# Kernel optimization log

Measured on AMD Instinct MI355X. Metric: run time of the kernel, lower is better.

Reference implementation:

```python
import jax, jax.numpy as jnp
import numpy as np

B, S, SK = 4, 256, 512
D, NH, NKV, HD = 1024, 16, 4, 64
DE, NE = 4096, 8
LANG_CODES = jnp.arange(4, 4 + NE)  # expert language codes (codes > 3 are routed)
LN_EPS = 1e-5


def setup_inputs() -> dict:
    key = jax.random.key(0)
    ks = jax.random.split(key, 32)
    sc = 0.02
    n = lambda k, shape: jax.random.normal(k, shape, jnp.float32)
    causal = jnp.where(jnp.tril(jnp.ones((S, S), bool)), 0.0, -1e9).astype(jnp.float32)
    inp = {
        "hidden_states": n(ks[0], (B, S, D)),
        "encoder_hidden_states": n(ks[1], (B, SK, D)),
        "attention_mask": jnp.broadcast_to(causal, (B, 1, S, S)),
        "encoder_attention_mask": jnp.zeros((B, 1, S, SK), jnp.float32),
        "langs": jax.random.randint(ks[2], (B, 2), 0, 12),
        "ln1_g": jnp.ones((D,), jnp.float32), "ln1_b": jnp.zeros((D,), jnp.float32),
        "sa_q_w": n(ks[3], (D, D)) * sc, "sa_q_b": jnp.zeros((D,), jnp.float32),
        "sa_k_w": n(ks[4], (D, NKV * HD)) * sc, "sa_k_b": jnp.zeros((NKV * HD,), jnp.float32),
        "sa_v_w": n(ks[5], (D, NKV * HD)) * sc, "sa_v_b": jnp.zeros((NKV * HD,), jnp.float32),
        "sa_o_w": n(ks[6], (D, D)) * sc, "sa_o_b": jnp.zeros((D,), jnp.float32),
        "ln2_g": jnp.ones((D,), jnp.float32), "ln2_b": jnp.zeros((D,), jnp.float32),
        "ca_q_w": n(ks[7], (D, D)) * sc, "ca_q_b": jnp.zeros((D,), jnp.float32),
        "ca_k_w": n(ks[8], (D, NKV * HD)) * sc, "ca_k_b": jnp.zeros((NKV * HD,), jnp.float32),
        "ca_v_w": n(ks[9], (D, NKV * HD)) * sc, "ca_v_b": jnp.zeros((NKV * HD,), jnp.float32),
        "ca_o_w": n(ks[10], (D, D)) * sc, "ca_o_b": jnp.zeros((D,), jnp.float32),
        "ln3_g": jnp.ones((D,), jnp.float32), "ln3_b": jnp.zeros((D,), jnp.float32),
        "moe_w1": n(ks[11], (NE, D, DE)) * sc,
        "moe_w2": n(ks[12], (NE, DE, D)) * sc,
        "moe_w3": n(ks[13], (NE, D, DE)) * sc,
    }
    return inp


def _ln(x, g, b):
    m = jnp.mean(x, -1, keepdims=True)
    v = jnp.var(x, -1, keepdims=True)
    return (x - m) * jax.lax.rsqrt(v + LN_EPS) * g + b


def _gqa(x, kv, qw, qb, kw, kb, vw, vb, ow, ob, mask):
    b, sq, _ = x.shape
    skv = kv.shape[1]
    q = ((x @ qw + qb) * HD ** -0.5).reshape(b, sq, NH, HD)
    k = (kv @ kw + kb).reshape(b, skv, NKV, HD)
    v = (kv @ vw + vb).reshape(b, skv, NKV, HD)
    rep = NH // NKV
    k = jnp.repeat(k, rep, axis=2)  # head h = kv_head*rep + r, matches repeat_kv
    v = jnp.repeat(v, rep, axis=2)
    scores = jnp.einsum('bqhd,bkhd->bhqk', q, k) + mask
    p = jax.nn.softmax(scores, axis=-1)
    o = jnp.einsum('bhqk,bkhd->bqhd', p, v).reshape(b, sq, NH * HD)
    return o @ ow + ob


def _moe(x, w1, w2, w3, langs):
    # routing: weight 1/(# lang codes > 3) per sequence; 1 if none
    counts = jnp.sum(langs > 3, axis=-1)
    rw = jnp.where(counts == 0, 1.0, 1.0 / jnp.maximum(counts, 1).astype(x.dtype))  # [B]
    match = jnp.any(langs[None, :, :] == LANG_CODES[:, None, None], axis=-1)  # [E,B]
    coef = match.astype(x.dtype) * rw[None, :]  # [E,B]
    h = jax.nn.gelu(jnp.einsum('bsd,edf->ebsf', x, w1), approximate=False) \
        * jnp.einsum('bsd,edf->ebsf', x, w3)
    out = jnp.einsum('ebsf,efd->ebsd', h, w2)
    return jnp.einsum('ebsd,eb->bsd', out, coef)


def reference(hidden_states, encoder_hidden_states, attention_mask, encoder_attention_mask,
              langs, ln1_g, ln1_b, sa_q_w, sa_q_b, sa_k_w, sa_k_b, sa_v_w, sa_v_b,
              sa_o_w, sa_o_b, ln2_g, ln2_b, ca_q_w, ca_q_b, ca_k_w, ca_k_b, ca_v_w,
              ca_v_b, ca_o_w, ca_o_b, ln3_g, ln3_b, moe_w1, moe_w2, moe_w3):
    # self attention (causal GQA, prefill, pre-LN)
    r = hidden_states
    h = _ln(hidden_states, ln1_g, ln1_b)
    h = _gqa(h, h, sa_q_w, sa_q_b, sa_k_w, sa_k_b, sa_v_w, sa_v_b, sa_o_w, sa_o_b,
             attention_mask)
    h = r + h
    # cross attention over encoder states
    r = h
    h = _ln(h, ln2_g, ln2_b)
    h = _gqa(h, encoder_hidden_states, ca_q_w, ca_q_b, ca_k_w, ca_k_b, ca_v_w, ca_v_b,
             ca_o_w, ca_o_b, encoder_attention_mask)
    h = r + h
    # language-routed MoE FFN
    r = h
    h = _ln(h, ln3_g, ln3_b)
    h = _moe(h, moe_w1, moe_w2, moe_w3, langs)
    return r + h
```

## Files before the change

### kernel.cpp

```cpp
#include <hip/hip_runtime.h>
#include <math.h>

#define B_   4
#define S_   256
#define SK_  512
#define D_   1024
#define NH_  16
#define NKV_ 4
#define HD_  64
#define DE_  4096
#define NE_  8

typedef __attribute__((ext_vector_type(8))) short bf16x8;
typedef __attribute__((ext_vector_type(4))) float f32x4;

struct __align__(8) s4 { short x, y, z, w; };

#define MFMA(a,b,c) __builtin_amdgcn_mfma_f32_16x16x32_bf16(a,b,c,0,0,0)

__device__ __forceinline__ unsigned short f2b(float f) {
  union { float f; unsigned u; } v; v.f = f;
  unsigned r = v.u + 0x7FFF + ((v.u >> 16) & 1);
  return (unsigned short)(r >> 16);
}

__device__ __forceinline__ unsigned short f2bh(float f) {
  return (unsigned short)((__float_as_uint(f) + 0x8000u) >> 16);
}

__device__ __forceinline__ void tconv_tile(float (*T)[65],
                                           const float* __restrict__ W,
                                           short* __restrict__ Wt,
                                           int N, int K, int n0, int k0) {
  int t = threadIdx.x;
  int kk = t >> 4, n4 = (t & 15) * 4;
#pragma unroll
  for (int it = 0; it < 4; ++it) {
    float4 v = *(const float4*)(W + (size_t)(k0 + kk + 16 * it) * N + n0 + n4);
    T[kk + 16 * it][n4 + 0] = v.x;
    T[kk + 16 * it][n4 + 1] = v.y;
    T[kk + 16 * it][n4 + 2] = v.z;
    T[kk + 16 * it][n4 + 3] = v.w;
  }
  __syncthreads();
  int n = t >> 2, kb = (t & 3) * 16;
  bf16x8 o0, o1;
#pragma unroll
  for (int j = 0; j < 8; ++j) o0[j] = (short)f2bh(T[kb + j][n]);
#pragma unroll
  for (int j = 0; j < 8; ++j) o1[j] = (short)f2bh(T[kb + 8 + j][n]);
  short* dst = Wt + (size_t)(n0 + n) * K + k0 + kb;
  *(bf16x8*)dst = o0;
  *(bf16x8*)(dst + 8) = o1;
}

struct P8 {
  const float* s[8];
  short* d[8];
  int n[8];
};

__global__ __launch_bounds__(256) void tconv_attn(P8 p) {
  int z = blockIdx.z;
  int N = p.n[z];
  if ((int)blockIdx.x * 64 >= N) return;
  __shared__ float T[64][65];
  tconv_tile(T, p.s[z], p.d[z], N, D_, blockIdx.x * 64, blockIdx.y * 64);
}

__global__ __launch_bounds__(256) void tconv_moe(const float* __restrict__ w1,
                                                 const float* __restrict__ w3,
                                                 const float* __restrict__ w2,
                                                 short* __restrict__ w1t,
                                                 short* __restrict__ w3t,
                                                 short* __restrict__ w2t,
                                                 const int* __restrict__ eact) {
  int z = blockIdx.z;
  int e = z / 3, m = z - e * 3;
  if (!eact[e]) return;
  __shared__ float T[64][65];
  size_t off = (size_t)e * D_ * DE_;
  if (m == 0) {
    tconv_tile(T, w1 + off, w1t + off, DE_, D_, blockIdx.x * 64, blockIdx.y * 64);
  } else if (m == 1) {
    tconv_tile(T, w3 + off, w3t + off, DE_, D_, blockIdx.x * 64, blockIdx.y * 64);
  } else {
    int lin = blockIdx.y * 64 + blockIdx.x;
    int nt = lin & 15, kt = lin >> 4;
    tconv_tile(T, w2 + off, w2t + off, D_, DE_, nt * 64, kt * 64);
  }
}

__global__ __launch_bounds__(256) void ln_kernel(const float* __restrict__ x,
                                                 const float* __restrict__ g,
                                                 const float* __restrict__ be,
                                                 short* __restrict__ y) {
  int row = blockIdx.x, tid = threadIdx.x;
  const float4 v = ((const float4*)(x + (size_t)row * D_))[tid];
  float s  = v.x + v.y + v.z + v.w;
  float s2 = v.x*v.x + v.y*v.y + v.z*v.z + v.w*v.w;
  __shared__ float r1[256], r2[256];
  r1[tid] = s; r2[tid] = s2; __syncthreads();
  for (int off = 128; off > 0; off >>= 1) {
    if (tid < off) { r1[tid] += r1[tid+off]; r2[tid] += r2[tid+off]; }
    __syncthreads();
  }
  float mean = r1[0] * (1.0f / D_);
  float var  = r2[0] * (1.0f / D_) - mean * mean;
  float inv  = rsqrtf(var + 1e-5f);
  int c = tid * 4;
  s4 o;
  o.x = (short)f2b((v.x - mean) * inv * g[c]   + be[c]);
  o.y = (short)f2b((v.y - mean) * inv * g[c+1] + be[c+1]);
  o.z = (short)f2b((v.z - mean) * inv * g[c+2] + be[c+2]);
  o.w = (short)f2b((v.w - mean) * inv * g[c+3] + be[c+3]);
  *(s4*)(y + (size_t)row * D_ + c) = o;
}

__global__ void cast_f2b(const float* __restrict__ in, short* __restrict__ out, int n) {
  int i = (blockIdx.x * 256 + threadIdx.x) * 4;
  if (i < n) {
    float4 v = *(const float4*)(in + i);
    s4 o; o.x=(short)f2b(v.x); o.y=(short)f2b(v.y); o.z=(short)f2b(v.z); o.w=(short)f2b(v.w);
    *(s4*)(out + i) = o;
  }
}

__global__ __launch_bounds__(256) void proj_mfma(const short* __restrict__ A,
                                                 const short* __restrict__ Wt,
                                                 const float* __restrict__ bias,
                                                 short* __restrict__ Cb,
                                                 float scale, int N, int K) {
  int bn = blockIdx.x * 64, bm = blockIdx.y * 64;
  int lane = threadIdx.x & 63, wv = threadIdx.x >> 6;
  int wm = (wv & 1) * 32, wn = (wv >> 1) * 32;
  int quad = lane >> 4, l16 = lane & 15;
  f32x4 z4 = {0.f,0.f,0.f,0.f};
  f32x4 acc[2][2] = {{z4,z4},{z4,z4}};
  const short* a0p = A + (size_t)(bm + wm + l16) * K;
  const short* a1p = a0p + (size_t)16 * K;
  const short* w0p = Wt + (size_t)(bn + wn + l16) * K;
  const short* w1p = w0p + (size_t)16 * K;
#pragma unroll 2
  for (int k0 = 0; k0 < K; k0 += 32) {
    int ka = k0 + quad * 8;
    bf16x8 a0 = *(const bf16x8*)(a0p + ka);
    bf16x8 a1 = *(const bf16x8*)(a1p + ka);
    bf16x8 b0 = *(const bf16x8*)(w0p + ka);
    bf16x8 b1 = *(const bf16x8*)(w1p + ka);
    acc[0][0] = MFMA(a0, b0, acc[0][0]);
    acc[0][1] = MFMA(a0, b1, acc[0][1]);
    acc[1][0] = MFMA(a1, b0, acc[1][0]);
    acc[1][1] = MFMA(a1, b1, acc[1][1]);
  }
#pragma unroll
  for (int i = 0; i < 2; ++i)
#pragma unroll
    for (int j = 0; j < 2; ++j) {
      int n = bn + wn + j*16 + l16;
      float bs = bias[n];
#pragma unroll
      for (int r = 0; r < 4; ++r) {
        int m = bm + wm + i*16 + quad*4 + r;
        Cb[(size_t)m * N + n] = (short)f2b((acc[i][j][r] + bs) * scale);
      }
    }
}

__global__ __launch_bounds__(256) void proj_v_mfma(const short* __restrict__ A,
                                                   const short* __restrict__ Wt,
                                                   const float* __restrict__ bias,
                                                   short* __restrict__ vT,
                                                   int SKV, int K) {
  int bn = blockIdx.x * 64, bm = blockIdx.y * 64;
  int lane = threadIdx.x & 63, wv = threadIdx.x >> 6;
  int wm = (wv & 1) * 32, wn = (wv >> 1) * 32;
  int quad = lane >> 4, l16 = lane & 15;
  f32x4 z4 = {0.f,0.f,0.f,0.f};
  f32x4 acc[2][2] = {{z4,z4},{z4,z4}};
  const short* a0p = A + (size_t)(bm + wm + l16) * K;
  const short* a1p = a0p + (size_t)16 * K;
  const short* w0p = Wt + (size_t)(bn + wn + l16) * K;
  const short* w1p = w0p + (size_t)16 * K;
#pragma unroll 2
  for (int k0 = 0; k0 < K; k0 += 32) {
    int ka = k0 + quad * 8;
    bf16x8 a0 = *(const bf16x8*)(a0p + ka);
    bf16x8 a1 = *(const bf16x8*)(a1p + ka);
    bf16x8 b0 = *(const bf16x8*)(w0p + ka);
    bf16x8 b1 = *(const bf16x8*)(w1p + ka);
    acc[0][0] = MFMA(a0, b0, acc[0][0]);
    acc[0][1] = MFMA(a0, b1, acc[0][1]);
    acc[1][0] = MFMA(a1, b0, acc[1][0]);
    acc[1][1] = MFMA(a1, b1, acc[1][1]);
  }
  __shared__ float T[64][65];
#pragma unroll
  for (int i = 0; i < 2; ++i)
#pragma unroll
    for (int j = 0; j < 2; ++j) {
      int nl = wn + j*16 + l16;
      float bs = bias[bn + nl];
#pragma unroll
      for (int r = 0; r < 4; ++r)
        T[nl][wm + i*16 + quad*4 + r] = acc[i][j][r] + bs;
    }
  __syncthreads();
  int t = threadIdx.x;
  int nl = t >> 2, m4 = (t & 3) * 16;
  int bb = bm / SKV, skv0 = bm % SKV;
  short* dst = vT + ((size_t)bb * 256 + bn + nl) * 512 + skv0 + m4;
  bf16x8 o0, o1;
#pragma unroll
  for (int ii = 0; ii < 8; ++ii) o0[ii] = (short)f2b(T[nl][m4 + ii]);
#pragma unroll
  for (int ii = 0; ii < 8; ++ii) o1[ii] = (short)f2b(T[nl][m4 + 8 + ii]);
  *(bf16x8*)dst = o0;
  *(bf16x8*)(dst + 8) = o1;
}

__global__ __launch_bounds__(256) void proj_o_mfma(const short* __restrict__ A,
                                                   const short* __restrict__ Wt,
                                                   const float* __restrict__ bias,
                                                   const float* __restrict__ rin,
                                                   float* __restrict__ C, int N, int K) {
  int bn = blockIdx.x * 64, bm = blockIdx.y * 64;
  int lane = threadIdx.x & 63, wv = threadIdx.x >> 6;
  int wm = (wv & 1) * 32, wn = (wv >> 1) * 32;
  int quad = lane >> 4, l16 = lane & 15;
  f32x4 z4 = {0.f,0.f,0.f,0.f};
  f32x4 acc[2][2] = {{z4,z4},{z4,z4}};
  const short* a0p = A + (size_t)(bm + wm + l16) * K;
  const short* a1p = a0p + (size_t)16 * K;
  const short* w0p = Wt + (size_t)(bn + wn + l16) * K;
  const short* w1p = w0p + (size_t)16 * K;
#pragma unroll 2
  for (int k0 = 0; k0 < K; k0 += 32) {
    int ka = k0 + quad * 8;
    bf16x8 a0 = *(const bf16x8*)(a0p + ka);
    bf16x8 a1 = *(const bf16x8*)(a1p + ka);
    bf16x8 b0 = *(const bf16x8*)(w0p + ka);
    bf16x8 b1 = *(const bf16x8*)(w1p + ka);
    acc[0][0] = MFMA(a0, b0, acc[0][0]);
    acc[0][1] = MFMA(a0, b1, acc[0][1]);
    acc[1][0] = MFMA(a1, b0, acc[1][0]);
    acc[1][1] = MFMA(a1, b1, acc[1][1]);
  }
#pragma unroll
  for (int i = 0; i < 2; ++i)
#pragma unroll
    for (int j = 0; j < 2; ++j) {
      int n = bn + wn + j*16 + l16;
      float bs = bias[n];
#pragma unroll
      for (int r = 0; r < 4; ++r) {
        int m = bm + wm + i*16 + quad*4 + r;
        C[(size_t)m * N + n] = acc[i][j][r] + bs + rin[(size_t)m * N + n];
      }
    }
}

__global__ __launch_bounds__(256) void qk_mfma(const short* __restrict__ Q,
                                               const short* __restrict__ Kb,
                                               const float* __restrict__ mask,
                                               float* __restrict__ sc,
                                               int b0, int SKV) {
  int z = blockIdx.z, zb = z >> 4, h = z & 15, b = b0 + zb, kvh = h >> 2;
  int bk = blockIdx.x * 64, bq = blockIdx.y * 64;
  int lane = threadIdx.x & 63, wv = threadIdx.x >> 6;
  int wm = (wv & 1) * 32, wn = (wv >> 1) * 32;
  int quad = lane >> 4, l16 = lane & 15;
  f32x4 z4 = {0.f,0.f,0.f,0.f};
  f32x4 acc[2][2] = {{z4,z4},{z4,z4}};
  const short* q0 = Q + (size_t)(b*S_ + bq + wm + l16) * D_ + h * HD_;
  const short* q1 = q0 + (size_t)16 * D_;
  const short* k0p = Kb + (size_t)(b*SKV + bk + wn + l16) * (NKV_*HD_) + kvh * HD_;
  const short* k1p = k0p + (size_t)16 * (NKV_*HD_);
#pragma unroll
  for (int d0 = 0; d0 < HD_; d0 += 32) {
    int ka = d0 + quad * 8;
    bf16x8 a0 = *(const bf16x8*)(q0 + ka);
    bf16x8 a1 = *(const bf16x8*)(q1 + ka);
    bf16x8 b0f = *(const bf16x8*)(k0p + ka);
    bf16x8 b1f = *(const bf16x8*)(k1p + ka);
    acc[0][0] = MFMA(a0, b0f, acc[0][0]);
    acc[0][1] = MFMA(a0, b1f, acc[0][1]);
    acc[1][0] = MFMA(a1, b0f, acc[1][0]);
    acc[1][1] = MFMA(a1, b1f, acc[1][1]);
  }
#pragma unroll
  for (int i = 0; i < 2; ++i)
#pragma unroll
    for (int j = 0; j < 2; ++j) {
      int n = bk + wn + j*16 + l16;
#pragma unroll
      for (int r = 0; r < 4; ++r) {
        int m = bq + wm + i*16 + quad*4 + r;
        sc[((size_t)(zb*NH_ + h) * S_ + m) * SKV + n] =
            acc[i][j][r] + mask[((size_t)(b*S_ + m)) * SKV + n];
      }
    }
}

__global__ __launch_bounds__(256) void softmax_kernel(float* __restrict__ sc, int SKV, int nrows) {
  int row = blockIdx.x * 4 + (threadIdx.x >> 6);
  int lane = threadIdx.x & 63;
  if (row >= nrows) return;
  float* rp = sc + (size_t)row * SKV;
  short* sp = (short*)rp;
  float4 v[2];
  int nc = SKV >> 8;
  float mx = -1e30f;
#pragma unroll
  for (int c = 0; c < 2; ++c)
    if (c < nc) {
      v[c] = *(float4*)(rp + c*256 + lane*4);
      mx = fmaxf(mx, fmaxf(fmaxf(v[c].x, v[c].y), fmaxf(v[c].z, v[c].w)));
    }
#pragma unroll
  for (int m = 32; m > 0; m >>= 1) mx = fmaxf(mx, __shfl_xor(mx, m, 64));
  float ls = 0.f;
#pragma unroll
  for (int c = 0; c < 2; ++c)
    if (c < nc) {
      v[c].x = __expf(v[c].x - mx); v[c].y = __expf(v[c].y - mx);
      v[c].z = __expf(v[c].z - mx); v[c].w = __expf(v[c].w - mx);
      ls += v[c].x + v[c].y + v[c].z + v[c].w;
    }
#pragma unroll
  for (int m = 32; m > 0; m >>= 1) ls += __shfl_xor(ls, m, 64);
  float inv = 1.0f / ls;
#pragma unroll
  for (int c = 0; c < 2; ++c)
    if (c < nc) {
      s4 o;
      o.x = (short)f2b(v[c].x * inv); o.y = (short)f2b(v[c].y * inv);
      o.z = (short)f2b(v[c].z * inv); o.w = (short)f2b(v[c].w * inv);
      *(s4*)(sp + c*256 + lane*4) = o;
    }
}

__global__ __launch_bounds__(256) void pv_mfma(const short* __restrict__ Pb,
                                               const short* __restrict__ vT,
                                               short* __restrict__ ob,
                                               int b0, int SKV) {
  int z = blockIdx.y, zb = z >> 4, h = z & 15, b = b0 + zb, kvh = h >> 2;
  int bq = blockIdx.x * 64;
  int lane = threadIdx.x & 63, wv = threadIdx.x >> 6;
  int wm = (wv & 1) * 32, wn = (wv >> 1) * 32;
  int quad = lane >> 4, l16 = lane & 15;
  f32x4 z4 = {0.f,0.f,0.f,0.f};
  f32x4 acc[2][2] = {{z4,z4},{z4,z4}};
  const short* p0 = Pb + ((size_t)(zb*NH_ + h) * S_ + bq + wm + l16) * (size_t)(2*SKV);
  const short* p1 = p0 + (size_t)16 * 2 * SKV;
  const short* v0 = vT + ((size_t)b * 256 + kvh*64 + wn + l16) * 512;
  const short* v1 = v0 + (size_t)16 * 512;
#pragma unroll 4
  for (int k0 = 0; k0 < SKV; k0 += 32) {
    int ka = k0 + quad * 8;
    bf16x8 a0 = *(const bf16x8*)(p0 + ka);
    bf16x8 a1 = *(const bf16x8*)(p1 + ka);
    bf16x8 b0f = *(const bf16x8*)(v0 + ka);
    bf16x8 b1f = *(const bf16x8*)(v1 + ka);
    acc[0][0] = MFMA(a0, b0f, acc[0][0]);
    acc[0][1] = MFMA(a0, b1f, acc[0][1]);
    acc[1][0] = MFMA(a1, b0f, acc[1][0]);
    acc[1][1] = MFMA(a1, b1f, acc[1][1]);
  }
#pragma unroll
  for (int i = 0; i < 2; ++i)
#pragma unroll
    for (int j = 0; j < 2; ++j) {
      int n = wn + j*16 + l16;
#pragma unroll
      for (int r = 0; r < 4; ++r) {
        int m = bq + wm + i*16 + quad*4 + r;
        ob[(size_t)(b*S_ + m) * D_ + h*HD_ + n] = (short)f2b(acc[i][j][r]);
      }
    }
}

__global__ __launch_bounds__(256) void moe_gate_mfma(const short* __restrict__ xlnb,
                                                     const short* __restrict__ w1t,
                                                     const short* __restrict__ w3t,
                                                     short* __restrict__ Hs,
                                                     const float* __restrict__ coef,
                                                     const int* __restrict__ slot) {
  int e = blockIdx.z;
  int bn = blockIdx.x * 64, bm = blockIdx.y * 64;
  int b = bm >> 8;
  if (coef[e * B_ + b] == 0.0f) return;
  int sl = slot[e * B_ + b];
  int lane = threadIdx.x & 63, wv = threadIdx.x >> 6;
  int wm = (wv & 1) * 32, wn = (wv >> 1) * 32;
  int quad = lane >> 4, l16 = lane & 15;
  f32x4 z4 = {0.f,0.f,0.f,0.f};
  f32x4 acc1[2][2] = {{z4,z4},{z4,z4}};
  f32x4 acc3[2][2] = {{z4,z4},{z4,z4}};
  size_t eoff = (size_t)e * D_ * DE_;
  const short* a0p = xlnb + (size_t)(bm + wm + l16) * D_;
  const short* a1p = a0p + (size_t)16 * D_;
  const short* w1p0 = w1t + eoff + (size_t)(bn + wn + l16) * D_;
  const short* w1p1 = w1p0 + (size_t)16 * D_;
  const short* w3p0 = w3t + eoff + (size_t)(bn + wn + l16) * D_;
  const short* w3p1 = w3p0 + (size_t)16 * D_;
#pragma unroll 2
  for (int k0 = 0; k0 < D_; k0 += 32) {
    int ka = k0 + quad * 8;
    bf16x8 a0 = *(const bf16x8*)(a0p + ka);
    bf16x8 a1 = *(const bf16x8*)(a1p + ka);
    bf16x8 b10 = *(const bf16x8*)(w1p0 + ka);
    bf16x8 b11 = *(const bf16x8*)(w1p1 + ka);
    bf16x8 b30 = *(const bf16x8*)(w3p0 + ka);
    bf16x8 b31 = *(const bf16x8*)(w3p1 + ka);
    acc1[0][0] = MFMA(a0, b10, acc1[0][0]);
    acc1[0][1] = MFMA(a0, b11, acc1[0][1]);
    acc1[1][0] = MFMA(a1, b10, acc1[1][0]);
    acc1[1][1] = MFMA(a1, b11, acc1[1][1]);
    acc3[0][0] = MFMA(a0, b30, acc3[0][0]);
    acc3[0][1] = MFMA(a0, b31, acc3[0][1]);
    acc3[1][0] = MFMA(a1, b30, acc3[1][0]);
    acc3[1][1] = MFMA(a1, b31, acc3[1][1]);
  }
  short* Hp = Hs + ((size_t)(sl * B_ + b) * S_ + (bm & 255)) * DE_;
#pragma unroll
  for (int i = 0; i < 2; ++i)
#pragma unroll
    for (int j = 0; j < 2; ++j) {
      int n = bn + wn + j*16 + l16;
#pragma unroll
      for (int r = 0; r < 4; ++r) {
        int lm = wm + i*16 + quad*4 + r;
        float c1 = acc1[i][j][r], c3 = acc3[i][j][r];
        float g = 0.5f * c1 * (1.0f + erff(c1 * 0.70710678118654752f));
        Hp[(size_t)lm * DE_ + n] = (short)f2b(g * c3);
      }
    }
}

__global__ __launch_bounds__(256) void moe_down_mfma(const short* __restrict__ Hs,
                                                     const short* __restrict__ w2t,
                                                     float* resid,
                                                     const float* __restrict__ coef,
                                                     const int* __restrict__ slot) {
  int zc = blockIdx.z;
  int e = zc >> 2, kc = zc & 3;
  int bn = blockIdx.x * 64, bm = blockIdx.y * 64;
  int b = bm >> 8;
  float cf = coef[e * B_ + b];
  if (cf == 0.0f) return;
  int sl = slot[e * B_ + b];
  int lane = threadIdx.x & 63, wv = threadIdx.x >> 6;
  int wm = (wv & 1) * 32, wn = (wv >> 1) * 32;
  int quad = lane >> 4, l16 = lane & 15;
  f32x4 z4 = {0.f,0.f,0.f,0.f};
  f32x4 acc[2][2] = {{z4,z4},{z4,z4}};
  const short* a0p = Hs + ((size_t)(sl * B_ + b) * S_ + (bm & 255) + wm + l16) * DE_ + kc * 1024;
  const short* a1p = a0p + (size_t)16 * DE_;
  const short* w0p = w2t + (size_t)e * DE_ * D_ + (size_t)(bn + wn + l16) * DE_ + kc * 1024;
  const short* w1p = w0p + (size_t)16 * DE_;
#pragma unroll 2
  for (int k0 = 0; k0 < 1024; k0 += 32) {
    int ka = k0 + quad * 8;
    bf16x8 a0 = *(const bf16x8*)(a0p + ka);
    bf16x8 a1 = *(const bf16x8*)(a1p + ka);
    bf16x8 b0 = *(const bf16x8*)(w0p + ka);
    bf16x8 b1 = *(const bf16x8*)(w1p + ka);
    acc[0][0] = MFMA(a0, b0, acc[0][0]);
    acc[0][1] = MFMA(a0, b1, acc[0][1]);
    acc[1][0] = MFMA(a1, b0, acc[1][0]);
    acc[1][1] = MFMA(a1, b1, acc[1][1]);
  }
#pragma unroll
  for (int i = 0; i < 2; ++i)
#pragma unroll
    for (int j = 0; j < 2; ++j) {
      int n = bn + wn + j*16 + l16;
#pragma unroll
      for (int r = 0; r < 4; ++r) {
        int m = bm + wm + i*16 + quad*4 + r;
        atomicAdd(&resid[(size_t)m * D_ + n], cf * acc[i][j][r]);
      }
    }
}

__global__ void coef_kernel(const int* __restrict__ langs, float* __restrict__ coef,
                            int* __restrict__ slot, int* __restrict__ eact) {
  int t = threadIdx.x;
  if (t < NE_ * B_) {
    int e = t >> 2, b = t & 3;
    int l0 = langs[b*2], l1 = langs[b*2 + 1];
    int counts = (l0 > 3) + (l1 > 3);
    float rw = (counts == 0) ? 1.0f : 1.0f / (float)counts;
    bool m = (l0 == 4 + e) || (l1 == 4 + e);
    coef[t] = m ? rw : 0.0f;
    int s = 0;
    for (int ep = 0; ep < e; ++ep) s += ((l0 == 4 + ep) || (l1 == 4 + ep)) ? 1 : 0;
    slot[t] = s;
  }
  if (t < NE_) {
    int any = 0;
    for (int b = 0; b < B_; ++b) {
      int l0 = langs[b*2], l1 = langs[b*2 + 1];
      any |= (l0 == 4 + t) || (l1 == 4 + t);
    }
    eact[t] = any;
  }
}

extern "C" void kernel_launch(void* const* d_in, const int* in_sizes, int n_in,
                              void* d_out, int out_size, void* d_ws, size_t ws_size,
                              hipStream_t stream) {
  const float* hidden = (const float*)d_in[0];
  const float* enc    = (const float*)d_in[1];
  const float* amask  = (const float*)d_in[2];
  const float* emask  = (const float*)d_in[3];
  const int*   langs  = (const int*)d_in[4];
  const float* ln1g = (const float*)d_in[5];
  const float* ln1b = (const float*)d_in[6];
  const float* saqw = (const float*)d_in[7];
  const float* saqb = (const float*)d_in[8];
  const float* sakw = (const float*)d_in[9];
  const float* sakb = (const float*)d_in[10];
  const float* savw = (const float*)d_in[11];
  const float* savb = (const float*)d_in[12];
  const float* saow = (const float*)d_in[13];
  const float* saob = (const float*)d_in[14];
  const float* ln2g = (const float*)d_in[15];
  const float* ln2b = (const float*)d_in[16];
  const float* caqw = (const float*)d_in[17];
  const float* caqb = (const float*)d_in[18];
  const float* cakw = (const float*)d_in[19];
  const float* cakb = (const float*)d_in[20];
  const float* cavw = (const float*)d_in[21];
  const float* cavb = (const float*)d_in[22];
  const float* caow = (const float*)d_in[23];
  const float* caob = (const float*)d_in[24];
  const float* ln3g = (const float*)d_in[25];
  const float* ln3b = (const float*)d_in[26];
  const float* w1   = (const float*)d_in[27];
  const float* w2   = (const float*)d_in[28];
  const float* w3   = (const float*)d_in[29];

  float* resid = (float*)d_out;

  const int M = B_ * S_;
  float* ws = (float*)d_ws;
  short* xlnb = (short*)ws;  ws += (M * D_) / 2;
  short* encb = (short*)ws;  ws += (B_ * SK_ * D_) / 2;
  short* qb   = (short*)ws;  ws += (M * D_) / 2;
  short* kb   = (short*)ws;  ws += (B_ * SK_ * 256) / 2;
  short* vT   = (short*)ws;  ws += (B_ * 256 * 512) / 2;
  short* ab   = (short*)ws;  ws += (M * D_) / 2;
  float* scb  = ws;          ws += B_ * NH_ * S_ * SK_;
  float* coef = ws;          ws += 32;
  int*   slot = (int*)ws;    ws += 32;
  int*   eact = (int*)ws;    ws += 32;
  short* saqt = (short*)ws;  ws += (D_ * D_) / 2;
  short* sakt = (short*)ws;  ws += (D_ * 256) / 2;
  short* savt = (short*)ws;  ws += (D_ * 256) / 2;
  short* saot = (short*)ws;  ws += (D_ * D_) / 2;
  short* caqt = (short*)ws;  ws += (D_ * D_) / 2;
  short* cakt = (short*)ws;  ws += (D_ * 256) / 2;
  short* cavt = (short*)ws;  ws += (D_ * 256) / 2;
  short* caot = (short*)ws;  ws += (D_ * D_) / 2;
  short* w1t  = (short*)ws;  ws += (size_t)NE_ * D_ * DE_ / 2;
  short* w3t  = (short*)ws;  ws += (size_t)NE_ * D_ * DE_ / 2;
  short* w2t  = (short*)ws;  ws += (size_t)NE_ * D_ * DE_ / 2;
  short* Hs   = (short*)scb;

  dim3 blk(256);

  P8 p;
  p.s[0] = saqw; p.d[0] = saqt; p.n[0] = D_;
  p.s[1] = sakw; p.d[1] = sakt; p.n[1] = 256;
  p.s[2] = savw; p.d[2] = savt; p.n[2] = 256;
  p.s[3] = saow; p.d[3] = saot; p.n[3] = D_;
  p.s[4] = caqw; p.d[4] = caqt; p.n[4] = D_;
  p.s[5] = cakw; p.d[5] = cakt; p.n[5] = 256;
  p.s[6] = cavw; p.d[6] = cavt; p.n[6] = 256;
  p.s[7] = caow; p.d[7] = caot; p.n[7] = D_;
  tconv_attn<<<dim3(16, 16, 8), blk, 0, stream>>>(p);
  coef_kernel<<<1, 64, 0, stream>>>(langs, coef, slot, eact);
  tconv_moe<<<dim3(64, 16, NE_ * 3), blk, 0, stream>>>(w1, w3, w2, w1t, w3t, w2t, eact);

  ln_kernel<<<M, blk, 0, stream>>>(hidden, ln1g, ln1b, xlnb);
  proj_mfma<<<dim3(16, 16), blk, 0, stream>>>(xlnb, saqt, saqb, qb, 0.125f, D_, D_);
  proj_mfma<<<dim3(4, 16), blk, 0, stream>>>(xlnb, sakt, sakb, kb, 1.0f, 256, D_);
  proj_v_mfma<<<dim3(4, 16), blk, 0, stream>>>(xlnb, savt, savb, vT, 256, D_);
  qk_mfma<<<dim3(4, 4, 4*NH_), blk, 0, stream>>>(qb, kb, amask, scb, 0, S_);
  softmax_kernel<<<(4*NH_*S_)/4, blk, 0, stream>>>(scb, S_, 4*NH_*S_);
  pv_mfma<<<dim3(4, 4*NH_), blk, 0, stream>>>((short*)scb, vT, ab, 0, S_);
  proj_o_mfma<<<dim3(16, 16), blk, 0, stream>>>(ab, saot, saob, hidden, resid, D_, D_);

  ln_kernel<<<M, blk, 0, stream>>>(resid, ln2g, ln2b, xlnb);
  proj_mfma<<<dim3(16, 16), blk, 0, stream>>>(xlnb, caqt, caqb, qb, 0.125f, D_, D_);
  cast_f2b<<<(B_*SK_*D_)/1024, blk, 0, stream>>>(enc, encb, B_*SK_*D_);
  proj_mfma<<<dim3(4, 32), blk, 0, stream>>>(encb, cakt, cakb, kb, 1.0f, 256, D_);
  proj_v_mfma<<<dim3(4, 32), blk, 0, stream>>>(encb, cavt, cavb, vT, 512, D_);
  qk_mfma<<<dim3(8, 4, 4*NH_), blk, 0, stream>>>(qb, kb, emask, scb, 0, SK_);
  softmax_kernel<<<(4*NH_*S_)/4, blk, 0, stream>>>(scb, SK_, 4*NH_*S_);
  pv_mfma<<<dim3(4, 4*NH_), blk, 0, stream>>>((short*)scb, vT, ab, 0, SK_);
  proj_o_mfma<<<dim3(16, 16), blk, 0, stream>>>(ab, caot, caob, resid, resid, D_, D_);

  ln_kernel<<<M, blk, 0, stream>>>(resid, ln3g, ln3b, xlnb);
  moe_gate_mfma<<<dim3(DE_/64, M/64, NE_), blk, 0, stream>>>(xlnb, w1t, w3t, Hs, coef, slot);
  moe_down_mfma<<<dim3(D_/64, M/64, NE_*4), blk, 0, stream>>>(Hs, w2t, resid, coef, slot);
}
```

Before: 834.1 us.

## Stage MoE GEMM tiles through double-buffered LDS with wider 64x128 tiles

Rewrites the MoE gate and down GEMM kernels so tiles are loaded into double-buffered shared memory with direct global-to-LDS loads, and overlaps the next tile's load with the current tile's MFMAs. Block tiles widen from 64x64 to 64x128, so each wave computes 32x64 and reuses A fragments across four B fragments. The aim is to cut redundant global loads, since the old kernels reloaded operands from global memory per wave without sharing. The cost is a barrier per k-step, more LDS, and more accumulator registers, which may lower occupancy and leaves fewer blocks for the small M.

```diff
diff --git a/kernel.cpp b/kernel.cpp
--- a/kernel.cpp
+++ b/kernel.cpp
@@ -387,51 +387,79 @@
                                                      const float* __restrict__ coef,
                                                      const int* __restrict__ slot) {
   int e = blockIdx.z;
-  int bn = blockIdx.x * 64, bm = blockIdx.y * 64;
+  int bn = blockIdx.x * 128, bm = blockIdx.y * 64;
   int b = bm >> 8;
   if (coef[e * B_ + b] == 0.0f) return;
   int sl = slot[e * B_ + b];
   int lane = threadIdx.x & 63, wv = threadIdx.x >> 6;
-  int wm = (wv & 1) * 32, wn = (wv >> 1) * 32;
+  int wm = (wv & 1) * 32, wn = (wv >> 1) * 64;
   int quad = lane >> 4, l16 = lane & 15;
+  int r4 = lane >> 2, c4 = lane & 3;
+
+  __shared__ short ldsA[2][64 * 32];
+  __shared__ short ldsB1[2][128 * 32];
+  __shared__ short ldsB3[2][128 * 32];
+
+  size_t eoff = (size_t)e * D_ * DE_;
+  const short* gA  = xlnb + (size_t)(bm + wv * 16 + r4) * D_ + c4 * 8;
+  const short* gB1 = w1t + eoff + (size_t)(bn + wv * 32 + r4) * D_ + c4 * 8;
+  const short* gB3 = w3t + eoff + (size_t)(bn + wv * 32 + r4) * D_ + c4 * 8;
+
   f32x4 z4 = {0.f,0.f,0.f,0.f};
-  f32x4 acc1[2][2] = {{z4,z4},{z4,z4}};
-  f32x4 acc3[2][2] = {{z4,z4},{z4,z4}};
-  size_t eoff = (size_t)e * D_ * DE_;
-  const short* a0p = xlnb + (size_t)(bm + wm + l16) * D_;
-  const short* a1p = a0p + (size_t)16 * D_;
-  const short* w1p0 = w1t + eoff + (size_t)(bn + wn + l16) * D_;
-  const short* w1p1 = w1p0 + (size_t)16 * D_;
-  const short* w3p0 = w3t + eoff + (size_t)(bn + wn + l16) * D_;
-  const short* w3p1 = w3p0 + (size_t)16 * D_;
-#pragma unroll 2
-  for (int k0 = 0; k0 < D_; k0 += 32) {
-    int ka = k0 + quad * 8;
-    bf16x8 a0 = *(const bf16x8*)(a0p + ka);
-    bf16x8 a1 = *(const bf16x8*)(a1p + ka);
-    bf16x8 b10 = *(const bf16x8*)(w1p0 + ka);
-    bf16x8 b11 = *(const bf16x8*)(w1p1 + ka);
-    bf16x8 b30 = *(const bf16x8*)(w3p0 + ka);
-    bf16x8 b31 = *(const bf16x8*)(w3p1 + ka);
-    acc1[0][0] = MFMA(a0, b10, acc1[0][0]);
-    acc1[0][1] = MFMA(a0, b11, acc1[0][1]);
-    acc1[1][0] = MFMA(a1, b10, acc1[1][0]);
-    acc1[1][1] = MFMA(a1, b11, acc1[1][1]);
-    acc3[0][0] = MFMA(a0, b30, acc3[0][0]);
-    acc3[0][1] = MFMA(a0, b31, acc3[0][1]);
-    acc3[1][0] = MFMA(a1, b30, acc3[1][0]);
-    acc3[1][1] = MFMA(a1, b31, acc3[1][1]);
-  }
+  f32x4 acc1[2][4] = {{z4,z4,z4,z4},{z4,z4,z4,z4}};
+  f32x4 acc3[2][4] = {{z4,z4,z4,z4},{z4,z4,z4,z4}};
+
+#define GATE_STAGE(cc, k0)                                                              \
+  do {                                                                                  \
+    __builtin_amdgcn_global_load_lds(gA + (k0),                 &ldsA[cc][wv*512], 16, 0, 0);  \
+    __builtin_amdgcn_global_load_lds(gB1 + (k0),                &ldsB1[cc][wv*1024], 16, 0, 0);\
+    __builtin_amdgcn_global_load_lds(gB1 + (size_t)16*D_ + (k0), &ldsB1[cc][wv*1024+512], 16, 0, 0);\
+    __builtin_amdgcn_global_load_lds(gB3 + (k0),                &ldsB3[cc][wv*1024], 16, 0, 0);\
+    __builtin_amdgcn_global_load_lds(gB3 + (size_t)16*D_ + (k0), &ldsB3[cc][wv*1024+512], 16, 0, 0);\
+  } while (0)
+
+#define GATE_COMP(cc)                                                                   \
+  do {                                                                                  \
+    bf16x8 a[2], f1[4], f3[4];                                                          \
+    a[0] = *(const bf16x8*)&ldsA[cc][(wm + l16) * 32 + quad * 8];                       \
+    a[1] = *(const bf16x8*)&ldsA[cc][(wm + 16 + l16) * 32 + quad * 8];                  \
+    _Pragma("unroll")                                                                   \
+    for (int ni = 0; ni < 4; ++ni) {                                                    \
+      f1[ni] = *(const bf16x8*)&ldsB1[cc][(wn + ni*16 + l16) * 32 + quad * 8];          \
+      f3[ni] = *(const bf16x8*)&ldsB3[cc][(wn + ni*16 + l16) * 32 + quad * 8];          \
+    }                                                                                   \
+    _Pragma("unroll")                                                                   \
+    for (int mi = 0; mi < 2; ++mi)                                                      \
+      _Pragma("unroll")                                                                 \
+      for (int ni = 0; ni < 4; ++ni) {                                                  \
+        acc1[mi][ni] = MFMA(a[mi], f1[ni], acc1[mi][ni]);                               \
+        acc3[mi][ni] = MFMA(a[mi], f3[ni], acc3[mi][ni]);                               \
+      }                                                                                 \
+  } while (0)
+
+  GATE_STAGE(0, 0);
+  __syncthreads();
+  int cur = 0;
+  for (int t = 0; t < (D_ / 32) - 1; ++t) {
+    GATE_STAGE(cur ^ 1, (t + 1) * 32);
+    GATE_COMP(cur);
+    __syncthreads();
+    cur ^= 1;
+  }
+  GATE_COMP(cur);
+#undef GATE_STAGE
+#undef GATE_COMP
+
   short* Hp = Hs + ((size_t)(sl * B_ + b) * S_ + (bm & 255)) * DE_;
 #pragma unroll
-  for (int i = 0; i < 2; ++i)
-#pragma unroll
-    for (int j = 0; j < 2; ++j) {
-      int n = bn + wn + j*16 + l16;
+  for (int mi = 0; mi < 2; ++mi)
+#pragma unroll
+    for (int ni = 0; ni < 4; ++ni) {
+      int n = bn + wn + ni * 16 + l16;
 #pragma unroll
       for (int r = 0; r < 4; ++r) {
-        int lm = wm + i*16 + quad*4 + r;
-        float c1 = acc1[i][j][r], c3 = acc3[i][j][r];
+        int lm = wm + mi * 16 + quad * 4 + r;
+        float c1 = acc1[mi][ni][r], c3 = acc3[mi][ni][r];
         float g = 0.5f * c1 * (1.0f + erff(c1 * 0.70710678118654752f));
         Hp[(size_t)lm * DE_ + n] = (short)f2b(g * c3);
       }
@@ -445,41 +473,71 @@
                                                      const int* __restrict__ slot) {
   int zc = blockIdx.z;
   int e = zc >> 2, kc = zc & 3;
-  int bn = blockIdx.x * 64, bm = blockIdx.y * 64;
+  int bn = blockIdx.x * 128, bm = blockIdx.y * 64;
   int b = bm >> 8;
   float cf = coef[e * B_ + b];
   if (cf == 0.0f) return;
   int sl = slot[e * B_ + b];
   int lane = threadIdx.x & 63, wv = threadIdx.x >> 6;
-  int wm = (wv & 1) * 32, wn = (wv >> 1) * 32;
+  int wm = (wv & 1) * 32, wn = (wv >> 1) * 64;
   int quad = lane >> 4, l16 = lane & 15;
+  int r4 = lane >> 2, c4 = lane & 3;
+
+  __shared__ short ldsA[2][64 * 32];
+  __shared__ short ldsB[2][128 * 32];
+
+  const short* gA = Hs + ((size_t)(sl * B_ + b) * S_ + (bm & 255) + wv * 16 + r4) * DE_
+                    + kc * 1024 + c4 * 8;
+  const short* gB = w2t + (size_t)e * DE_ * D_ + (size_t)(bn + wv * 32 + r4) * DE_
+                    + kc * 1024 + c4 * 8;
+
   f32x4 z4 = {0.f,0.f,0.f,0.f};
-  f32x4 acc[2][2] = {{z4,z4},{z4,z4}};
-  const short* a0p = Hs + ((size_t)(sl * B_ + b) * S_ + (bm & 255) + wm + l16) * DE_ + kc * 1024;
-  const short* a1p = a0p + (size_t)16 * DE_;
-  const short* w0p = w2t + (size_t)e * DE_ * D_ + (size_t)(bn + wn + l16) * DE_ + kc * 1024;
-  const short* w1p = w0p + (size_t)16 * DE_;
-#pragma unroll 2
-  for (int k0 = 0; k0 < 1024; k0 += 32) {
-    int ka = k0 + quad * 8;
-    bf16x8 a0 = *(const bf16x8*)(a0p + ka);
-    bf16x8 a1 = *(const bf16x8*)(a1p + ka);
-    bf16x8 b0 = *(const bf16x8*)(w0p + ka);
-    bf16x8 b1 = *(const bf16x8*)(w1p + ka);
-    acc[0][0] = MFMA(a0, b0, acc[0][0]);
-    acc[0][1] = MFMA(a0, b1, acc[0][1]);
-    acc[1][0] = MFMA(a1, b0, acc[1][0]);
-    acc[1][1] = MFMA(a1, b1, acc[1][1]);
-  }
-#pragma unroll
-  for (int i = 0; i < 2; ++i)
-#pragma unroll
-    for (int j = 0; j < 2; ++j) {
-      int n = bn + wn + j*16 + l16;
+  f32x4 acc[2][4] = {{z4,z4,z4,z4},{z4,z4,z4,z4}};
+
+#define DOWN_STAGE(cc, k0)                                                              \
+  do {                                                                                  \
+    __builtin_amdgcn_global_load_lds(gA + (k0),                  &ldsA[cc][wv*512], 16, 0, 0); \
+    __builtin_amdgcn_global_load_lds(gB + (k0),                  &ldsB[cc][wv*1024], 16, 0, 0);\
+    __builtin_amdgcn_global_load_lds(gB + (size_t)16*DE_ + (k0), &ldsB[cc][wv*1024+512], 16, 0, 0);\
+  } while (0)
+
+#define DOWN_COMP(cc)                                                                   \
+  do {                                                                                  \
+    bf16x8 a[2], f[4];                                                                  \
+    a[0] = *(const bf16x8*)&ldsA[cc][(wm + l16) * 32 + quad * 8];                       \
+    a[1] = *(const bf16x8*)&ldsA[cc][(wm + 16 + l16) * 32 + quad * 8];                  \
+    _Pragma("unroll")                                                                   \
+    for (int ni = 0; ni < 4; ++ni)                                                      \
+      f[ni] = *(const bf16x8*)&ldsB[cc][(wn + ni*16 + l16) * 32 + quad * 8];            \
+    _Pragma("unroll")                                                                   \
+    for (int mi = 0; mi < 2; ++mi)                                                      \
+      _Pragma("unroll")                                                                 \
+      for (int ni = 0; ni < 4; ++ni)                                                    \
+        acc[mi][ni] = MFMA(a[mi], f[ni], acc[mi][ni]);                                  \
+  } while (0)
+
+  DOWN_STAGE(0, 0);
+  __syncthreads();
+  int cur = 0;
+  for (int t = 0; t < 31; ++t) {
+    DOWN_STAGE(cur ^ 1, (t + 1) * 32);
+    DOWN_COMP(cur);
+    __syncthreads();
+    cur ^= 1;
+  }
+  DOWN_COMP(cur);
+#undef DOWN_STAGE
+#undef DOWN_COMP
+
+#pragma unroll
+  for (int mi = 0; mi < 2; ++mi)
+#pragma unroll
+    for (int ni = 0; ni < 4; ++ni) {
+      int n = bn + wn + ni * 16 + l16;
 #pragma unroll
       for (int r = 0; r < 4; ++r) {
-        int m = bm + wm + i*16 + quad*4 + r;
-        atomicAdd(&resid[(size_t)m * D_ + n], cf * acc[i][j][r]);
+        int m = bm + wm + mi * 16 + quad * 4 + r;
+        atomicAdd(&resid[(size_t)m * D_ + n], cf * acc[mi][ni][r]);
       }
     }
 }
@@ -604,6 +662,6 @@
   proj_o_mfma<<<dim3(16, 16), blk, 0, stream>>>(ab, caot, caob, resid, resid, D_, D_);
 
   ln_kernel<<<M, blk, 0, stream>>>(resid, ln3g, ln3b, xlnb);
-  moe_gate_mfma<<<dim3(DE_/64, M/64, NE_), blk, 0, stream>>>(xlnb, w1t, w3t, Hs, coef, slot);
-  moe_down_mfma<<<dim3(D_/64, M/64, NE_*4), blk, 0, stream>>>(Hs, w2t, resid, coef, slot);
-}
+  moe_gate_mfma<<<dim3(DE_/128, M/64, NE_), blk, 0, stream>>>(xlnb, w1t, w3t, Hs, coef, slot);
+  moe_down_mfma<<<dim3(D_/128, M/64, NE_*4), blk, 0, stream>>>(Hs, w2t, resid, coef, slot);
+}
```

Result: faster. 729.4 us (-12.6%).
